# Kernel tuning notes

Hardware: AMD Instinct MI355X
Metric: run time of the kernel (lower is better)

The kernel has to match this reference:

```python
import jax, jax.numpy as jnp
import numpy as np

N = 50000
E = 1600000
IN_C = 64
HID = 16
HEADS = 4
OUT_C = 1
ATT_SLOPE = 0.2   # GATConv negative_slope for attention logits
ACT_SLOPE = 0.01  # F.leaky_relu default between layers


def _glorot(key, shape):
    fan_in, fan_out = shape[0], shape[-1]
    lim = jnp.sqrt(6.0 / (fan_in + fan_out))
    return jax.random.uniform(key, shape, jnp.float32, -lim, lim)


def setup_inputs() -> dict:
    key = jax.random.key(0)
    ks = jax.random.split(key, 12)
    x = jax.random.normal(ks[0], (N, IN_C), jnp.float32)
    edge_index = jax.random.randint(ks[1], (2, E), 0, N, jnp.int64)
    return {
        "x": x,
        "edge_index": edge_index,
        # GAT layer 1: in -> HID per head, HEADS heads (concat)
        "W1": _glorot(ks[2], (IN_C, HEADS * HID)),
        "att_src1": _glorot(ks[3], (HEADS, HID)),
        "att_dst1": _glorot(ks[4], (HEADS, HID)),
        "b1": jnp.zeros((HEADS * HID,), jnp.float32),
        # GAT layer 2: HEADS*HID -> HID, 1 head
        "W2": _glorot(ks[5], (HEADS * HID, HID)),
        "att_src2": _glorot(ks[6], (1, HID)),
        "att_dst2": _glorot(ks[7], (1, HID)),
        "b2": jnp.zeros((HID,), jnp.float32),
        # final linear
        "Wo": _glorot(ks[8], (HID, OUT_C)),
        "bo": jnp.zeros((OUT_C,), jnp.float32),
    }


def _gat_layer(x, src, dst, W, a_src, a_dst, b, n_nodes):
    """PyG GATConv (eval mode): h = xW; edge logits from additive attention;
    segment softmax over incoming edges of each dst; weighted scatter-sum."""
    H, C = a_src.shape
    h = (x @ W).reshape(n_nodes, H, C)                       # [N, H, C]
    alpha_s = jnp.einsum("nhc,hc->nh", h, a_src)             # [N, H]
    alpha_d = jnp.einsum("nhc,hc->nh", h, a_dst)             # [N, H]
    e = jax.nn.leaky_relu(alpha_s[src] + alpha_d[dst], ATT_SLOPE)  # [E, H]
    m = jax.ops.segment_max(e, dst, num_segments=n_nodes)    # [N, H]
    w = jnp.exp(e - m[dst])
    denom = jax.ops.segment_sum(w, dst, num_segments=n_nodes)
    alpha = w / denom[dst]                                   # [E, H] (self-loops => denom>0)
    out = jax.ops.segment_sum(h[src] * alpha[:, :, None], dst, num_segments=n_nodes)
    return out.reshape(n_nodes, H * C) + b                   # concat heads + bias


def reference(x, edge_index, W1, att_src1, att_dst1, b1,
              W2, att_src2, att_dst2, b2, Wo, bo):
    n = x.shape[0]
    loops = jnp.arange(n, dtype=edge_index.dtype)
    src = jnp.concatenate([edge_index[0], loops])            # add_self_loops=True
    dst = jnp.concatenate([edge_index[1], loops])
    h = _gat_layer(x, src, dst, W1, att_src1, att_dst1, b1, n)
    h = jax.nn.leaky_relu(h, ACT_SLOPE)
    h = _gat_layer(h, src, dst, W2, att_src2, att_dst2, b2, n)
    h = jax.nn.leaky_relu(h, ACT_SLOPE)
    return h @ Wo + bo                                       # [N, 1]
```

## Files before the change

kernel.cpp:

```cpp
#include <hip/hip_runtime.h>
#include <hip/hip_bf16.h>
#include <cstdint>

#define N_NODES 50000
#define N_EDGES 1600000
#define EE (N_EDGES + N_NODES)
#define BSH 7
#define BSIZE 128
#define NBUCKET ((N_NODES + BSIZE - 1) >> BSH)
#define CSH 13
#define CAP 8192
#define BIN_BLOCKS 403
#define GEMM_BLOCKS 3125


__device__ __forceinline__ float lrelu(float x, float s) { return x >= 0.f ? x : s * x; }
__device__ __forceinline__ float bflo(uint32_t v) { return __uint_as_float(v << 16); }
__device__ __forceinline__ float bfhi(uint32_t v) { return __uint_as_float(v & 0xFFFF0000u); }
__device__ __forceinline__ uint32_t packbf(float a, float b) {
    uint32_t ua = __float_as_uint(a), ub = __float_as_uint(b);
    ua += 0x7FFF + ((ua >> 16) & 1);
    ub += 0x7FFF + ((ub >> 16) & 1);
    return (ua >> 16) | (ub & 0xFFFF0000u);
}
__device__ __forceinline__ float rdlane(float v, int l) {
    return __uint_as_float(__builtin_amdgcn_readlane(__float_as_uint(v), l));
}

__global__ __launch_bounds__(256) void k_pre(
    const float* __restrict__ x, const float* __restrict__ W1,
    const float* __restrict__ as_w, const float* __restrict__ ad_w,
    uint32_t* __restrict__ h1b, float* __restrict__ as1, float* __restrict__ ad1,
    const int* __restrict__ src, const int* __restrict__ dst,
    int* __restrict__ bcur, uint32_t* __restrict__ binned) {
    if (blockIdx.x < BIN_BLOCKS) {
        __shared__ int lcnt[NBUCKET];
        __shared__ int lbase[NBUCKET];
        const int T = 16;
        for (int i = threadIdx.x; i < NBUCKET; i += 256) lcnt[i] = 0;
        __syncthreads();
        uint32_t pv[T];
        uint32_t pm[T];
        int base = blockIdx.x * (256 * T);
        if (base + 256 * T <= N_EDGES) {
            const int4* s4 = (const int4*)(src + base);
            const int4* d4 = (const int4*)(dst + base);
#pragma unroll
            for (int k = 0; k < 4; k++) {
                int4 sv = s4[threadIdx.x + k * 256];
                int4 dv = d4[threadIdx.x + k * 256];
                int ss[4] = {sv.x, sv.y, sv.z, sv.w};
                int dd[4] = {dv.x, dv.y, dv.z, dv.w};
#pragma unroll
                for (int j = 0; j < 4; j++) {
                    int b = dd[j] >> BSH;
                    int r = atomicAdd(&lcnt[b], 1);
                    pv[k * 4 + j] = (uint32_t)ss[j] | ((uint32_t)(dd[j] & (BSIZE - 1)) << 16);
                    pm[k * 4 + j] = (uint32_t)r | ((uint32_t)b << 16);
                }
            }
        } else {
#pragma unroll
            for (int k = 0; k < T; k++) {
                int e = base + ((k & 3) * 4 + (k >> 2)) * 256 + threadIdx.x;
                pm[k] = 0xFFFFFFFFu;
                if (e < EE) {
                    int s, d;
                    if (e < N_EDGES) { s = src[e]; d = dst[e]; } else { s = e - N_EDGES; d = s; }
                    int b = d >> BSH;
                    int r = atomicAdd(&lcnt[b], 1);
                    pv[k] = (uint32_t)s | ((uint32_t)(d & (BSIZE - 1)) << 16);
                    pm[k] = (uint32_t)r | ((uint32_t)b << 16);
                }
            }
        }
        __syncthreads();
        for (int i = threadIdx.x; i < NBUCKET; i += 256) {
            int c = lcnt[i];
            if (c) lbase[i] = atomicAdd(&bcur[i], c);
        }
        __syncthreads();
#pragma unroll
        for (int k = 0; k < T; k++) {
            if (pm[k] != 0xFFFFFFFFu) {
                int b = pm[k] >> 16, r = pm[k] & 0xFFFF;
                binned[((size_t)b << CSH) + lbase[b] + r] = pv[k];
            }
        }
        return;
    }
    int c = threadIdx.x & 63;
    int wv = threadIdx.x >> 6;
    float wreg[64];
#pragma unroll
    for (int k = 0; k < 64; k++) wreg[k] = W1[k * 64 + c];
    float aw = as_w[c];
    float dw = ad_w[c];
    int base = (blockIdx.x - BIN_BLOCKS) * 16 + wv * 4;
#pragma unroll
    for (int r = 0; r < 4; r++) {
        int n = base + r;
        float xr = x[n * 64 + c];
        float a0 = 0.f, a1 = 0.f, a2 = 0.f, a3 = 0.f;
#pragma unroll
        for (int k = 0; k < 64; k += 4) {
            a0 = fmaf(rdlane(xr, k),     wreg[k],     a0);
            a1 = fmaf(rdlane(xr, k + 1), wreg[k + 1], a1);
            a2 = fmaf(rdlane(xr, k + 2), wreg[k + 2], a2);
            a3 = fmaf(rdlane(xr, k + 3), wreg[k + 3], a3);
        }
        float acc = (a0 + a1) + (a2 + a3);
        float other = __shfl_xor(acc, 1, 64);
        if (!(c & 1)) h1b[n * 32 + (c >> 1)] = packbf(acc, other);
        float asv = acc * aw;
        float adv = acc * dw;
#pragma unroll
        for (int off = 1; off < 16; off <<= 1) {
            asv += __shfl_xor(asv, off, 64);
            adv += __shfl_xor(adv, off, 64);
        }
        if ((c & 15) == 0) { as1[n * 4 + (c >> 4)] = asv; ad1[n * 4 + (c >> 4)] = adv; }
    }
}

__global__ __launch_bounds__(512) void kB_sort(const int* __restrict__ bcur, const uint32_t* __restrict__ binned,
                                               int* __restrict__ rowdesc, unsigned short* __restrict__ esrc) {
    int b = blockIdx.x, tid = threadIdx.x, wv = tid >> 6;
    int p0 = b << CSH;
    int L = bcur[b];
    __shared__ int cnt8[8][BSIZE];
    __shared__ int wbase[8][BSIZE];
    __shared__ int shs[BSIZE];
    for (int i = tid; i < 8 * BSIZE; i += 512) ((int*)cnt8)[i] = 0;
    __syncthreads();

    uint32_t pv[16];
    unsigned short rk[16];
#pragma unroll
    for (int k = 0; k < 16; k++) {
        int i = tid + k * 512;
        if (i < L) {
            uint32_t v = binned[p0 + i];
            pv[k] = v;
            rk[k] = (unsigned short)atomicAdd(&cnt8[wv][(v >> 16) & (BSIZE - 1)], 1);
        }
    }
    __syncthreads();

    int tot = 0;
    if (tid < BSIZE) {
#pragma unroll
        for (int w = 0; w < 8; w++) tot += cnt8[w][tid];
        shs[tid] = tot;
    }
    __syncthreads();
    if (tid < 64) {
        int t0 = shs[2 * tid], t1 = shs[2 * tid + 1];
        int pair = t0 + t1;
        int incl = pair;
#pragma unroll
        for (int off = 1; off < 64; off <<= 1) {
            int t = __shfl_up(incl, off, 64);
            if (tid >= off) incl += t;
        }
        int exclp = incl - pair;
        shs[2 * tid] = exclp;
        shs[2 * tid + 1] = exclp + t0;
    }
    __syncthreads();
    if (tid < BSIZE) {
        int excl = shs[tid];
        int node = (b << BSH) + tid;
        if (node < N_NODES) rowdesc[node] = excl | (tot << 13);
        int wb = excl;
#pragma unroll
        for (int w = 0; w < 8; w++) { wbase[w][tid] = wb; wb += cnt8[w][tid]; }
    }
    __syncthreads();

#pragma unroll
    for (int k = 0; k < 16; k++) {
        int i = tid + k * 512;
        if (i < L) {
            uint32_t v = pv[k];
            int dl = (v >> 16) & (BSIZE - 1);
            esrc[p0 + wbase[wv][dl] + (int)rk[k]] = (unsigned short)(v & 0xFFFF);
        }
    }
}

__global__ __launch_bounds__(256) void k_aggr1f(
    const int* __restrict__ rowdesc, const unsigned short* __restrict__ esrc,
    const float* __restrict__ as1, const float* __restrict__ ad1,
    const uint32_t* __restrict__ h1b,
    const float* __restrict__ b1, const float* __restrict__ W2,
    const float* __restrict__ as2w, const float* __restrict__ ad2w,
    uint32_t* __restrict__ h2b, float* __restrict__ as2, float* __restrict__ ad2) {
    int n = blockIdx.x * 4 + (threadIdx.x >> 6);
    int lane = threadIdx.x & 63;
    int md = rowdesc[n];
    int begin = ((n >> BSH) << CSH) + (md & (CAP - 1));
    int deg = md >> 13;

    int slot = lane >> 3, cl = lane & 7;
    int hc = cl >> 1;
    float ad1h = ad1[n * 4 + hc];

    const uint4* h1b4 = (const uint4*)h1b;
    float a0 = 0.f, a1 = 0.f, a2 = 0.f, a3 = 0.f, a4 = 0.f, a5 = 0.f, a6 = 0.f, a7 = 0.f, dsum = 0.f;

    int iters = (deg + 7) >> 3;
#pragma unroll 4
    for (int it = 0; it < iters; it++) {
        int idx = it * 8 + slot;
        bool ok = idx < deg;
        int s = ok ? (int)esrc[begin + idx] : 0;
        float e = as1[s * 4 + hc] + ad1h;
        float w = __expf(e >= 0.f ? e : 0.2f * e);
        w = ok ? w : 0.f;
        uint4 v = h1b4[s * 8 + cl];
        dsum += w;
        a0 += w * bflo(v.x); a1 += w * bfhi(v.x);
        a2 += w * bflo(v.y); a3 += w * bfhi(v.y);
        a4 += w * bflo(v.z); a5 += w * bfhi(v.z);
        a6 += w * bflo(v.w); a7 += w * bfhi(v.w);
    }
#pragma unroll
    for (int off = 8; off <= 32; off <<= 1) {
        a0 += __shfl_xor(a0, off, 64); a1 += __shfl_xor(a1, off, 64);
        a2 += __shfl_xor(a2, off, 64); a3 += __shfl_xor(a3, off, 64);
        a4 += __shfl_xor(a4, off, 64); a5 += __shfl_xor(a5, off, 64);
        a6 += __shfl_xor(a6, off, 64); a7 += __shfl_xor(a7, off, 64);
        dsum += __shfl_xor(dsum, off, 64);
    }
    float dinv = 1.f / dsum;

    float4 bb0 = *(const float4*)(b1 + 8 * cl);
    float4 bb1 = *(const float4*)(b1 + 8 * cl + 4);
    float act0 = lrelu(a0 * dinv + bb0.x, 0.01f);
    float act1 = lrelu(a1 * dinv + bb0.y, 0.01f);
    float act2 = lrelu(a2 * dinv + bb0.z, 0.01f);
    float act3 = lrelu(a3 * dinv + bb0.w, 0.01f);
    float act4 = lrelu(a4 * dinv + bb1.x, 0.01f);
    float act5 = lrelu(a5 * dinv + bb1.y, 0.01f);
    float act6 = lrelu(a6 * dinv + bb1.z, 0.01f);
    float act7 = lrelu(a7 * dinv + bb1.w, 0.01f);

    int co = lane & 15, kg = lane >> 4;
    int l0 = 2 * kg, l1 = 2 * kg + 1;
    const float* w2r = W2 + (16 * kg) * 16 + co;
    float g = 0.f;
    g = fmaf(__shfl(act0, l0, 64), w2r[0 * 16],  g);
    g = fmaf(__shfl(act1, l0, 64), w2r[1 * 16],  g);
    g = fmaf(__shfl(act2, l0, 64), w2r[2 * 16],  g);
    g = fmaf(__shfl(act3, l0, 64), w2r[3 * 16],  g);
    g = fmaf(__shfl(act4, l0, 64), w2r[4 * 16],  g);
    g = fmaf(__shfl(act5, l0, 64), w2r[5 * 16],  g);
    g = fmaf(__shfl(act6, l0, 64), w2r[6 * 16],  g);
    g = fmaf(__shfl(act7, l0, 64), w2r[7 * 16],  g);
    g = fmaf(__shfl(act0, l1, 64), w2r[8 * 16],  g);
    g = fmaf(__shfl(act1, l1, 64), w2r[9 * 16],  g);
    g = fmaf(__shfl(act2, l1, 64), w2r[10 * 16], g);
    g = fmaf(__shfl(act3, l1, 64), w2r[11 * 16], g);
    g = fmaf(__shfl(act4, l1, 64), w2r[12 * 16], g);
    g = fmaf(__shfl(act5, l1, 64), w2r[13 * 16], g);
    g = fmaf(__shfl(act6, l1, 64), w2r[14 * 16], g);
    g = fmaf(__shfl(act7, l1, 64), w2r[15 * 16], g);
    g += __shfl_xor(g, 16, 64);
    g += __shfl_xor(g, 32, 64);
    float godd = __shfl_xor(g, 1, 64);
    if (lane < 16 && !(lane & 1)) h2b[n * 8 + (lane >> 1)] = packbf(g, godd);
    float asv = g * as2w[co];
    float adv2 = g * ad2w[co];
#pragma unroll
    for (int off = 1; off < 16; off <<= 1) {
        asv += __shfl_xor(asv, off, 64);
        adv2 += __shfl_xor(adv2, off, 64);
    }
    if (lane == 0) { as2[n] = asv; ad2[n] = adv2; }
}

__global__ __launch_bounds__(256) void k_aggr2(
    const int* __restrict__ rowdesc, const unsigned short* __restrict__ esrc,
    const float* __restrict__ as2, const float* __restrict__ ad2,
    const uint32_t* __restrict__ h2b,
    const float* __restrict__ b2, const float* __restrict__ Wo,
    const float* __restrict__ bo, float* __restrict__ out) {
    int n = blockIdx.x * 4 + (threadIdx.x >> 6);
    int lane = threadIdx.x & 63;
    int md = rowdesc[n];
    int begin = ((n >> BSH) << CSH) + (md & (CAP - 1));
    int deg = md >> 13;
    float adv = ad2[n];

    int slot = lane >> 3, c2 = lane & 7;
    float acc0 = 0.f, acc1 = 0.f, dsum = 0.f;

    int iters = (deg + 7) >> 3;
#pragma unroll 4
    for (int it = 0; it < iters; it++) {
        int idx = it * 8 + slot;
        bool ok = idx < deg;
        int s = ok ? (int)esrc[begin + idx] : 0;
        float e = as2[s] + adv;
        float w = __expf(e >= 0.f ? e : 0.2f * e);
        w = ok ? w : 0.f;
        uint32_t hv = h2b[s * 8 + c2];
        acc0 += w * bflo(hv);
        acc1 += w * bfhi(hv);
        dsum += w;
    }
#pragma unroll
    for (int off = 8; off <= 32; off <<= 1) {
        acc0 += __shfl_xor(acc0, off, 64);
        acc1 += __shfl_xor(acc1, off, 64);
        dsum += __shfl_xor(dsum, off, 64);
    }
    float v0 = lrelu(acc0 / dsum + b2[2 * c2], 0.01f) * Wo[2 * c2];
    float v1 = lrelu(acc1 / dsum + b2[2 * c2 + 1], 0.01f) * Wo[2 * c2 + 1];
    float y = v0 + v1;
    y += __shfl_xor(y, 1, 64);
    y += __shfl_xor(y, 2, 64);
    y += __shfl_xor(y, 4, 64);
    if (lane == 0) out[n] = y + bo[0];
}

extern "C" void kernel_launch(void* const* d_in, const int* in_sizes, int n_in,
                              void* d_out, int out_size, void* d_ws, size_t ws_size,
                              hipStream_t stream) {
    const float* x    = (const float*)d_in[0];
    const int*   ei   = (const int*)d_in[1];
    const float* W1   = (const float*)d_in[2];
    const float* as1w = (const float*)d_in[3];
    const float* ad1w = (const float*)d_in[4];
    const float* b1   = (const float*)d_in[5];
    const float* W2   = (const float*)d_in[6];
    const float* as2w = (const float*)d_in[7];
    const float* ad2w = (const float*)d_in[8];
    const float* b2   = (const float*)d_in[9];
    const float* Wo   = (const float*)d_in[10];
    const float* bo   = (const float*)d_in[11];
    float* out = (float*)d_out;

    const int* srcp = ei;
    const int* dstp = ei + N_EDGES;

    char* p = (char*)d_ws;
    auto alloc = [&](size_t bytes) -> char* {
        char* r = p;
        p += (bytes + 255) / 256 * 256;
        return r;
    };
    int*            bcur    = (int*)alloc((size_t)(NBUCKET + 1) * 4);
    int*            rowdesc = (int*)alloc((size_t)N_NODES * 4);
    uint32_t*       binned  = (uint32_t*)alloc((size_t)NBUCKET * CAP * 4);
    unsigned short* esrc    = (unsigned short*)alloc((size_t)NBUCKET * CAP * 2 + 256);
    uint32_t*       h2b     = (uint32_t*)alloc((size_t)N_NODES * 8 * 4);
    uint32_t*       h1b     = (uint32_t*)alloc((size_t)N_NODES * 32 * 4);
    float*          as1     = (float*)alloc((size_t)N_NODES * 4 * 4);
    float*          ad1     = (float*)alloc((size_t)N_NODES * 4 * 4);
    float*          as2     = (float*)alloc((size_t)N_NODES * 4);
    float*          ad2     = (float*)alloc((size_t)N_NODES * 4);

    hipMemsetAsync(bcur, 0, (size_t)(NBUCKET + 1) * 4, stream);

    k_pre<<<BIN_BLOCKS + GEMM_BLOCKS, 256, 0, stream>>>(x, W1, as1w, ad1w, h1b, as1, ad1,
                                                        srcp, dstp, bcur, binned);
    kB_sort<<<NBUCKET, 512, 0, stream>>>(bcur, binned, rowdesc, esrc);
    k_aggr1f<<<N_NODES / 4, 256, 0, stream>>>(rowdesc, esrc, as1, ad1, h1b, b1, W2, as2w, ad2w,
                                              h2b, as2, ad2);
    k_aggr2<<<N_NODES / 4, 256, 0, stream>>>(rowdesc, esrc, as2, ad2, h2b, b2, Wo, bo, out);
}
```

Before: 194.1 us.

## Split layer-1 GEMM between binning kernel and sort kernel to balance load

Half of the per-node layer-1 projection (nodes past SPLIT) moves out of the binning/GEMM kernel into extra blocks appended to the bucket-sort kernel. The sort kernel has only about 391 blocks and likely underfills the GPU, so the extra GEMM blocks fill idle CUs while the first kernel gets shorter. The GEMM code is factored into a shared device helper. The sort kernel may now need more registers at 512 threads because of the 64-float weight array, which could lower its occupancy.

```diff
diff --git a/kernel.cpp b/kernel.cpp
--- a/kernel.cpp
+++ b/kernel.cpp
@@ -11,7 +11,9 @@
 #define CSH 13
 #define CAP 8192
 #define BIN_BLOCKS 403
-#define GEMM_BLOCKS 3125
+#define SPLIT 24992
+#define K1_GEMM_BLOCKS (SPLIT / 16)
+#define K2_GEMM_BLOCKS ((N_NODES - SPLIT + 31) / 32)
 
 
 __device__ __forceinline__ float lrelu(float x, float s) { return x >= 0.f ? x : s * x; }
@@ -25,6 +27,42 @@
 }
 __device__ __forceinline__ float rdlane(float v, int l) {
     return __uint_as_float(__builtin_amdgcn_readlane(__float_as_uint(v), l));
+}
+
+__device__ __forceinline__ void gemm1_wave(
+    int base, int c,
+    const float* __restrict__ x, const float* __restrict__ W1,
+    const float* __restrict__ as_w, const float* __restrict__ ad_w,
+    uint32_t* __restrict__ h1b, float* __restrict__ as1, float* __restrict__ ad1) {
+    float wreg[64];
+#pragma unroll
+    for (int k = 0; k < 64; k++) wreg[k] = W1[k * 64 + c];
+    float aw = as_w[c];
+    float dw = ad_w[c];
+#pragma unroll
+    for (int r = 0; r < 4; r++) {
+        int n = base + r;
+        float xr = x[n * 64 + c];
+        float a0 = 0.f, a1 = 0.f, a2 = 0.f, a3 = 0.f;
+#pragma unroll
+        for (int k = 0; k < 64; k += 4) {
+            a0 = fmaf(rdlane(xr, k),     wreg[k],     a0);
+            a1 = fmaf(rdlane(xr, k + 1), wreg[k + 1], a1);
+            a2 = fmaf(rdlane(xr, k + 2), wreg[k + 2], a2);
+            a3 = fmaf(rdlane(xr, k + 3), wreg[k + 3], a3);
+        }
+        float acc = (a0 + a1) + (a2 + a3);
+        float other = __shfl_xor(acc, 1, 64);
+        if (!(c & 1)) h1b[n * 32 + (c >> 1)] = packbf(acc, other);
+        float asv = acc * aw;
+        float adv = acc * dw;
+#pragma unroll
+        for (int off = 1; off < 16; off <<= 1) {
+            asv += __shfl_xor(asv, off, 64);
+            adv += __shfl_xor(adv, off, 64);
+        }
+        if ((c & 15) == 0) { as1[n * 4 + (c >> 4)] = asv; ad1[n * 4 + (c >> 4)] = adv; }
+    }
 }
 
 __global__ __launch_bounds__(256) void k_pre(
@@ -91,41 +129,26 @@
     }
     int c = threadIdx.x & 63;
     int wv = threadIdx.x >> 6;
-    float wreg[64];
-#pragma unroll
-    for (int k = 0; k < 64; k++) wreg[k] = W1[k * 64 + c];
-    float aw = as_w[c];
-    float dw = ad_w[c];
     int base = (blockIdx.x - BIN_BLOCKS) * 16 + wv * 4;
-#pragma unroll
-    for (int r = 0; r < 4; r++) {
-        int n = base + r;
-        float xr = x[n * 64 + c];
-        float a0 = 0.f, a1 = 0.f, a2 = 0.f, a3 = 0.f;
-#pragma unroll
-        for (int k = 0; k < 64; k += 4) {
-            a0 = fmaf(rdlane(xr, k),     wreg[k],     a0);
-            a1 = fmaf(rdlane(xr, k + 1), wreg[k + 1], a1);
-            a2 = fmaf(rdlane(xr, k + 2), wreg[k + 2], a2);
-            a3 = fmaf(rdlane(xr, k + 3), wreg[k + 3], a3);
-        }
-        float acc = (a0 + a1) + (a2 + a3);
-        float other = __shfl_xor(acc, 1, 64);
-        if (!(c & 1)) h1b[n * 32 + (c >> 1)] = packbf(acc, other);
-        float asv = acc * aw;
-        float adv = acc * dw;
-#pragma unroll
-        for (int off = 1; off < 16; off <<= 1) {
-            asv += __shfl_xor(asv, off, 64);
-            adv += __shfl_xor(adv, off, 64);
-        }
-        if ((c & 15) == 0) { as1[n * 4 + (c >> 4)] = asv; ad1[n * 4 + (c >> 4)] = adv; }
-    }
-}
-
-__global__ __launch_bounds__(512) void kB_sort(const int* __restrict__ bcur, const uint32_t* __restrict__ binned,
-                                               int* __restrict__ rowdesc, unsigned short* __restrict__ esrc) {
-    int b = blockIdx.x, tid = threadIdx.x, wv = tid >> 6;
+    gemm1_wave(base, c, x, W1, as_w, ad_w, h1b, as1, ad1);
+}
+
+__global__ __launch_bounds__(512) void kB_sort(
+    const int* __restrict__ bcur, const uint32_t* __restrict__ binned,
+    int* __restrict__ rowdesc, unsigned short* __restrict__ esrc,
+    const float* __restrict__ x, const float* __restrict__ W1,
+    const float* __restrict__ as_w, const float* __restrict__ ad_w,
+    uint32_t* __restrict__ h1b, float* __restrict__ as1, float* __restrict__ ad1) {
+    int tid = threadIdx.x;
+    if (blockIdx.x >= NBUCKET) {
+        int c = tid & 63;
+        int wv8 = tid >> 6;
+        int base = SPLIT + (blockIdx.x - NBUCKET) * 32 + wv8 * 4;
+        if (base >= N_NODES) return;
+        gemm1_wave(base, c, x, W1, as_w, ad_w, h1b, as1, ad1);
+        return;
+    }
+    int b = blockIdx.x, wv = tid >> 6;
     int p0 = b << CSH;
     int L = bcur[b];
     __shared__ int cnt8[8][BSIZE];
@@ -364,9 +387,10 @@
 
     hipMemsetAsync(bcur, 0, (size_t)(NBUCKET + 1) * 4, stream);
 
-    k_pre<<<BIN_BLOCKS + GEMM_BLOCKS, 256, 0, stream>>>(x, W1, as1w, ad1w, h1b, as1, ad1,
-                                                        srcp, dstp, bcur, binned);
-    kB_sort<<<NBUCKET, 512, 0, stream>>>(bcur, binned, rowdesc, esrc);
+    k_pre<<<BIN_BLOCKS + K1_GEMM_BLOCKS, 256, 0, stream>>>(x, W1, as1w, ad1w, h1b, as1, ad1,
+                                                           srcp, dstp, bcur, binned);
+    kB_sort<<<NBUCKET + K2_GEMM_BLOCKS, 512, 0, stream>>>(bcur, binned, rowdesc, esrc,
+                                                          x, W1, as1w, ad1w, h1b, as1, ad1);
     k_aggr1f<<<N_NODES / 4, 256, 0, stream>>>(rowdesc, esrc, as1, ad1, h1b, b1, W2, as2w, ad2w,
                                               h2b, as2, ad2);
     k_aggr2<<<N_NODES / 4, 256, 0, stream>>>(rowdesc, esrc, as2, ad2, h2b, b2, Wo, bo, out);
```

New measurement: 192.8 us. Within noise of the previous version (-0.7%).
